# Optimization experiments

Measured on AMD Instinct MI355X. Metric: run time of the kernel, lower is better.

## Reference

```python
import jax, jax.numpy as jnp
import numpy as np


def setup_inputs() -> dict:
    key = jax.random.key(0)
    k1, k2, k3, k4 = jax.random.split(key, 4)
    B, C_in, KH, KW, C_out = 256, 512, 7, 7, 1000
    inputR = jax.random.normal(k1, (B, C_in, KH, KW), dtype=jnp.float32)
    inputSPD = jax.random.normal(k2, (B, C_in, C_in), dtype=jnp.float32)
    fan_in = C_in * KH * KW
    weight = jax.random.normal(k3, (C_out, C_in, KH, KW), dtype=jnp.float32) / np.sqrt(fan_in)
    bias = jax.random.normal(k4, (C_out,), dtype=jnp.float32) / np.sqrt(fan_in)
    return {"inputR": inputR, "inputSPD": inputSPD, "weight": weight, "bias": bias}


def reference(inputR, inputSPD, weight, bias):
    # Conv2d with kernel == spatial size and padding 0 == fully connected layer.
    # outputR: (N, C_out)
    outputR = jnp.einsum('nchw,ochw->no', inputR, weight) + bias

    # top-2 channel selection per sample (indices only; values unused)
    _, top2_idx = jax.lax.top_k(outputR, 2)  # (N, 2)

    # weight is detached for the SPD path in the original module
    w_spd = jax.lax.stop_gradient(weight)[top2_idx]  # (N, 2, C_in, KH, KW)

    # outputSPD[n,k,m] = sum_{c,d,h,w} SPD[n,c,d] * W2[n,k,d,h,w] * W2[n,m,c,h,w]
    # (equivalent to the original's two batched matmuls + sum over (h, w))
    outputSPD = jnp.einsum('ncd,nkdhw,nmchw->nkm', inputSPD, w_spd, w_spd)  # (N, 2, 2)
    return outputR, outputSPD
```

## Files before the change

### kernel.cpp

```cpp
#include <hip/hip_runtime.h>

#define KD 25088
#define N_DIM 1000

typedef __attribute__((ext_vector_type(8))) short bf16x8;
typedef __attribute__((ext_vector_type(4))) float f32x4;

__device__ inline unsigned short f2bf(float x) {
  union { float f; unsigned u; } v; v.f = x;
  unsigned r = v.u + 0x7FFFu + ((v.u >> 16) & 1);
  return (unsigned short)(r >> 16);
}
__device__ inline unsigned pack2(float a, float b) {
  return (unsigned)f2bf(a) | ((unsigned)f2bf(b) << 16);
}
__device__ inline float bf2f(unsigned short u) {
  union { unsigned u; float f; } v; v.u = ((unsigned)u) << 16; return v.f;
}

__global__ __launch_bounds__(256) void init_bias_k(
    const float* __restrict__ bias, float* __restrict__ outR) {
  const int id = blockIdx.x * 256 + threadIdx.x;
  if (id < 256 * N_DIM) outR[id] = bias[id % N_DIM];
}

__global__ __launch_bounds__(256) void rgemm_k(
    const float* __restrict__ A, const float* __restrict__ W,
    float* __restrict__ outR) {
  __shared__ unsigned short As[2][128 * 32];
  __shared__ unsigned short Bs[2][128 * 32];
  const int t = threadIdx.x;
  const int m0 = blockIdx.x * 128;
  const int n0 = blockIdx.y * 128;
  const int z  = blockIdx.z;
  const int lane = t & 63, w = t >> 6;
  const int cw = (w >> 1) * 64, jw = (w & 1) * 64;
  const int r16 = lane & 15, quad = lane >> 4;
  const int srow = t >> 2;
  const int sc8  = (t & 3) << 3;

  float a_pre[16], b_pre[16];

  f32x4 acc[4][4];
#pragma unroll
  for (int i = 0; i < 4; ++i)
#pragma unroll
    for (int j = 0; j < 4; ++j) {
      acc[i][j][0] = 0.f; acc[i][j][1] = 0.f;
      acc[i][j][2] = 0.f; acc[i][j][3] = 0.f;
    }

#define RG_LOAD(s_)                                                         \
  {                                                                         \
    const int kbase = ((z) * 28 + (s_)) * 32;                               \
    _Pragma("unroll")                                                       \
    for (int h = 0; h < 2; ++h) {                                           \
      const int row = h * 64 + srow;                                        \
      const float* pa = A + (size_t)(m0 + row) * KD + kbase + sc8;          \
      *(float4*)&a_pre[h * 8 + 0] = *(const float4*)pa;                     \
      *(float4*)&a_pre[h * 8 + 4] = *(const float4*)(pa + 4);               \
      const int wr = n0 + row;                                              \
      if (wr < N_DIM) {                                                     \
        const float* pw = W + (size_t)wr * KD + kbase + sc8;                \
        *(float4*)&b_pre[h * 8 + 0] = *(const float4*)pw;                   \
        *(float4*)&b_pre[h * 8 + 4] = *(const float4*)(pw + 4);             \
      } else {                                                              \
        _Pragma("unroll")                                                   \
        for (int q = 0; q < 8; ++q) b_pre[h * 8 + q] = 0.f;                 \
      }                                                                     \
    }                                                                       \
  }

#define RG_WRITE(p_)                                                        \
  {                                                                         \
    _Pragma("unroll")                                                       \
    for (int h = 0; h < 2; ++h) {                                           \
      const int row = h * 64 + srow;                                        \
      uint4 ua, ub;                                                         \
      ua.x = pack2(a_pre[h*8+0], a_pre[h*8+1]);                             \
      ua.y = pack2(a_pre[h*8+2], a_pre[h*8+3]);                             \
      ua.z = pack2(a_pre[h*8+4], a_pre[h*8+5]);                             \
      ua.w = pack2(a_pre[h*8+6], a_pre[h*8+7]);                             \
      ub.x = pack2(b_pre[h*8+0], b_pre[h*8+1]);                             \
      ub.y = pack2(b_pre[h*8+2], b_pre[h*8+3]);                             \
      ub.z = pack2(b_pre[h*8+4], b_pre[h*8+5]);                             \
      ub.w = pack2(b_pre[h*8+6], b_pre[h*8+7]);                             \
      *(uint4*)&As[p_][row * 32 + sc8] = ua;                                \
      *(uint4*)&Bs[p_][row * 32 + sc8] = ub;                                \
    }                                                                       \
  }

  RG_LOAD(0); RG_WRITE(0); __syncthreads();
  int p = 0;
  for (int s = 0; s < 28; ++s) {
    if (s + 1 < 28) RG_LOAD(s + 1);
    bf16x8 af[4], bq[4];
#pragma unroll
    for (int i = 0; i < 4; ++i) {
      af[i] = *(const bf16x8*)&As[p][(cw + i * 16 + r16) * 32 + quad * 8];
      bq[i] = *(const bf16x8*)&Bs[p][(jw + i * 16 + r16) * 32 + quad * 8];
    }
#pragma unroll
    for (int i = 0; i < 4; ++i)
#pragma unroll
      for (int j = 0; j < 4; ++j)
        acc[i][j] = __builtin_amdgcn_mfma_f32_16x16x32_bf16(af[i], bq[j], acc[i][j], 0, 0, 0);
    if (s + 1 < 28) RG_WRITE(p ^ 1);
    __syncthreads();
    p ^= 1;
  }

#pragma unroll
  for (int j = 0; j < 4; ++j) {
    const int n = n0 + jw + j * 16 + r16;
    if (n < N_DIM) {
#pragma unroll
      for (int i = 0; i < 4; ++i)
#pragma unroll
        for (int r = 0; r < 4; ++r) {
          const int m = m0 + cw + i * 16 + quad * 4 + r;
          atomicAdd(&outR[(size_t)m * N_DIM + n], acc[i][j][r]);
        }
    }
  }
#undef RG_LOAD
#undef RG_WRITE
}

__global__ __launch_bounds__(64) void top8_k(
    const float* __restrict__ outR, int* __restrict__ top2,
    int* __restrict__ candIdx, int* __restrict__ flags,
    float* __restrict__ outSPD) {
  const int n = blockIdx.x;
  const int lane = threadIdx.x;
  float v[16];
#pragma unroll
  for (int r = 0; r < 16; ++r) {
    const int o = lane + r * 64;
    v[r] = (o < N_DIM) ? outR[n * N_DIM + o] : -3.0e38f;
  }
  float cv[8]; int ci[8];
#pragma unroll
  for (int rr = 0; rr < 8; ++rr) {
    float bv = -3.0e38f; int bi = 0x3fffffff;
#pragma unroll
    for (int r = 0; r < 16; ++r) {
      const int o = lane + r * 64;
      if (v[r] > bv || (v[r] == bv && o < bi)) { bv = v[r]; bi = o; }
    }
#pragma unroll
    for (int off = 32; off >= 1; off >>= 1) {
      const float ov = __shfl_xor(bv, off, 64);
      const int   oi = __shfl_xor(bi, off, 64);
      if (ov > bv || (ov == bv && oi < bi)) { bv = ov; bi = oi; }
    }
    cv[rr] = bv; ci[rr] = bi;
#pragma unroll
    for (int r = 0; r < 16; ++r)
      if (lane + r * 64 == bi) v[r] = -3.0e38f;
  }
  if (lane == 0) {
    const bool safe = (cv[0] - cv[1] >= 0.025f) &&
                      (cv[1] - cv[2] >= 0.025f) &&
                      (cv[1] - cv[7] >= 0.05f);
    flags[n] = safe ? 0 : 1;
    top2[2 * n]     = ci[0];
    top2[2 * n + 1] = ci[1];
#pragma unroll
    for (int r = 0; r < 8; ++r) candIdx[n * 8 + r] = ci[r];
    outSPD[4 * n + 0] = 0.f; outSPD[4 * n + 1] = 0.f;
    outSPD[4 * n + 2] = 0.f; outSPD[4 * n + 3] = 0.f;
  }
}

__global__ __launch_bounds__(256) void rdot_k(
    const float* __restrict__ A, const float* __restrict__ W,
    const float* __restrict__ bias, const int* __restrict__ candIdx,
    const int* __restrict__ flags, float* __restrict__ vals) {
  const int n = blockIdx.x;
  if (!flags[n]) return;
  const int c = blockIdx.y;
  const int idx = candIdx[n * 8 + c];
  const float4* a4 = (const float4*)(A + (size_t)n * KD);
  const float4* w4 = (const float4*)(W + (size_t)idx * KD);
  float s = 0.f;
  for (int i = threadIdx.x; i < KD / 4; i += 256) {
    const float4 av = a4[i];
    const float4 wv = w4[i];
    s += av.x * wv.x + av.y * wv.y + av.z * wv.z + av.w * wv.w;
  }
#pragma unroll
  for (int off = 32; off >= 1; off >>= 1) s += __shfl_xor(s, off, 64);
  __shared__ float red[4];
  const int lane = threadIdx.x & 63, w = threadIdx.x >> 6;
  if (lane == 0) red[w] = s;
  __syncthreads();
  if (threadIdx.x == 0)
    vals[n * 8 + c] = red[0] + red[1] + red[2] + red[3] + bias[idx];
}

__global__ __launch_bounds__(64) void select_k(
    const float* __restrict__ vals, const int* __restrict__ candIdx,
    const int* __restrict__ flags, int* __restrict__ top2) {
  const int n = blockIdx.x;
  if (threadIdx.x != 0 || !flags[n]) return;
  int b0 = -1; float v0 = -3.0e38f; int i0 = 0x3fffffff;
  for (int c = 0; c < 8; ++c) {
    const int idx = candIdx[n * 8 + c];
    const float vv = vals[n * 8 + c];
    if (vv > v0 || (vv == v0 && idx < i0)) { v0 = vv; i0 = idx; b0 = c; }
  }
  float v1 = -3.0e38f; int i1 = 0x3fffffff;
  for (int c = 0; c < 8; ++c) {
    if (c == b0) continue;
    const int idx = candIdx[n * 8 + c];
    const float vv = vals[n * 8 + c];
    if (vv > v1 || (vv == v1 && idx < i1)) { v1 = vv; i1 = idx; }
  }
  top2[2 * n]     = i0;
  top2[2 * n + 1] = i1;
}

__global__ __launch_bounds__(256) void pack_k(
    const float* __restrict__ W, const int* __restrict__ top2,
    unsigned short* __restrict__ Wp) {
  const int n  = blockIdx.x;
  const int jq = blockIdx.y;
  const int ia = top2[2 * n];
  const int ib = top2[2 * n + 1];
  unsigned short* dst = Wp + (size_t)n * 65536;
  for (int u = threadIdx.x; u < 32 * 256; u += 256) {
    const int j  = jq * 32 + (u >> 8);
    const int d2 = (u & 255) * 2;
    unsigned val = 0u;
    if (j < 98) {
      const int kk = (j >= 49);
      const int hw = j - 49 * kk;
      const float* wr = W + (size_t)(kk ? ib : ia) * KD + hw;
      val = pack2(wr[(size_t)d2 * 49], wr[(size_t)(d2 + 1) * 49]);
    }
    *(unsigned*)(dst + j * 512 + d2) = val;
  }
}

__global__ __launch_bounds__(256) void spd_k(
    const float* __restrict__ S, const unsigned short* __restrict__ Wp,
    float* __restrict__ outSPD) {
  __shared__ unsigned short As[2][128 * 32];
  __shared__ unsigned short Bs[2][128 * 32];
  __shared__ float red[4];
  const int t = threadIdx.x;
  const int n  = blockIdx.x >> 2;
  const int c0 = (blockIdx.x & 3) * 128;
  const float* Sn = S + (size_t)n * 512 * 512;
  const unsigned short* Wpn = Wp + (size_t)n * 65536;
  const int lane = t & 63, w = t >> 6;
  const int cw = (w >> 1) * 64, jw = (w & 1) * 64;
  const int r16 = lane & 15, quad = lane >> 4;
  const int srow = t >> 2;
  const int sc8  = (t & 3) << 3;

  if (t < 4) red[t] = 0.f;

  float a_pre[16];
  uint4 b_pre[2];

  f32x4 acc[4][4];
#pragma unroll
  for (int i = 0; i < 4; ++i)
#pragma unroll
    for (int j = 0; j < 4; ++j) {
      acc[i][j][0] = 0.f; acc[i][j][1] = 0.f;
      acc[i][j][2] = 0.f; acc[i][j][3] = 0.f;
    }

#define SP_LOAD(s_)                                                         \
  {                                                                         \
    const int d0 = (s_) * 32;                                               \
    _Pragma("unroll")                                                       \
    for (int h = 0; h < 2; ++h) {                                           \
      const int row = h * 64 + srow;                                        \
      const float* pa = Sn + (size_t)(c0 + row) * 512 + d0 + sc8;           \
      *(float4*)&a_pre[h * 8 + 0] = *(const float4*)pa;                     \
      *(float4*)&a_pre[h * 8 + 4] = *(const float4*)(pa + 4);               \
      b_pre[h] = *(const uint4*)(Wpn + (size_t)row * 512 + d0 + sc8);       \
    }                                                                       \
  }

#define SP_WRITE(p_)                                                        \
  {                                                                         \
    _Pragma("unroll")                                                       \
    for (int h = 0; h < 2; ++h) {                                           \
      const int row = h * 64 + srow;                                        \
      uint4 ua;                                                             \
      ua.x = pack2(a_pre[h*8+0], a_pre[h*8+1]);                             \
      ua.y = pack2(a_pre[h*8+2], a_pre[h*8+3]);                             \
      ua.z = pack2(a_pre[h*8+4], a_pre[h*8+5]);                             \
      ua.w = pack2(a_pre[h*8+6], a_pre[h*8+7]);                             \
      *(uint4*)&As[p_][row * 32 + sc8] = ua;                                \
      *(uint4*)&Bs[p_][row * 32 + sc8] = b_pre[h];                          \
    }                                                                       \
  }

  SP_LOAD(0); SP_WRITE(0); __syncthreads();
  int p = 0;
  for (int s = 0; s < 16; ++s) {
    if (s + 1 < 16) SP_LOAD(s + 1);
    bf16x8 af[4], bq[4];
#pragma unroll
    for (int i = 0; i < 4; ++i) {
      af[i] = *(const bf16x8*)&As[p][(cw + i * 16 + r16) * 32 + quad * 8];
      bq[i] = *(const bf16x8*)&Bs[p][(jw + i * 16 + r16) * 32 + quad * 8];
    }
#pragma unroll
    for (int i = 0; i < 4; ++i)
#pragma unroll
      for (int j = 0; j < 4; ++j)
        acc[i][j] = __builtin_amdgcn_mfma_f32_16x16x32_bf16(af[i], bq[j], acc[i][j], 0, 0, 0);
    if (s + 1 < 16) SP_WRITE(p ^ 1);
    __syncthreads();
    p ^= 1;
  }
#undef SP_LOAD
#undef SP_WRITE

  float p00 = 0.f, p01 = 0.f, p10 = 0.f, p11 = 0.f;
#pragma unroll
  for (int j = 0; j < 4; ++j) {
    const int jj = jw + j * 16 + r16;
    if (jj < 98) {
      const int kk = (jj >= 49);
      const int hw = jj - 49 * kk;
      const unsigned short* wa = Wpn + (size_t)hw * 512;
      const unsigned short* wb = Wpn + (size_t)(49 + hw) * 512;
#pragma unroll
      for (int i = 0; i < 4; ++i) {
#pragma unroll
        for (int r = 0; r < 4; ++r) {
          const int c = c0 + cw + i * 16 + quad * 4 + r;
          const float u   = acc[i][j][r];
          const float wav = bf2f(wa[c]);
          const float wbv = bf2f(wb[c]);
          if (kk == 0) { p00 = fmaf(u, wav, p00); p01 = fmaf(u, wbv, p01); }
          else         { p10 = fmaf(u, wav, p10); p11 = fmaf(u, wbv, p11); }
        }
      }
    }
  }

  atomicAdd(&red[0], p00);
  atomicAdd(&red[1], p01);
  atomicAdd(&red[2], p10);
  atomicAdd(&red[3], p11);
  __syncthreads();
  if (t < 4) atomicAdd(&outSPD[n * 4 + t], red[t]);
}

__global__ __launch_bounds__(256) void spd_fb_k(
    const float* __restrict__ S, const float* __restrict__ W,
    const int* __restrict__ top2, float* __restrict__ outSPD) {
  __shared__ unsigned short As[128 * 40];
  __shared__ unsigned short Bs[128 * 40];
  __shared__ float red[4];
  const int t = threadIdx.x;
  const int n  = blockIdx.x >> 2;
  const int c0 = (blockIdx.x & 3) * 128;
  const int ia = top2[2 * n];
  const int ib = top2[2 * n + 1];
  const float* Sn = S + (size_t)n * 512 * 512;
  const int lane = t & 63, w = t >> 6;
  const int cw = (w >> 1) * 64, jw = (w & 1) * 64;
  const int r16 = lane & 15, quad = lane >> 4;
  if (t < 4) red[t] = 0.f;
  f32x4 acc[4][4];
#pragma unroll
  for (int i = 0; i < 4; ++i)
#pragma unroll
    for (int j = 0; j < 4; ++j) {
      acc[i][j][0] = 0.f; acc[i][j][1] = 0.f;
      acc[i][j][2] = 0.f; acc[i][j][3] = 0.f;
    }
  const int bj  = t & 127;
  const int bh  = t >> 7;
  const int bkk = (bj >= 49);
  const int bhw = bj - 49 * bkk;
  const bool bvalid = (bj < 98);
  const float* brow = W + (size_t)(bkk ? ib : ia) * KD + bhw;
  for (int d0 = 0; d0 < 512; d0 += 32) {
#pragma unroll
    for (int h = 0; h < 4; ++h) {
      const int idx = h * 256 + t;
      const int row = idx >> 3;
      const int c4  = (idx & 7) << 2;
      float4 av = *(const float4*)(Sn + (size_t)(c0 + row) * 512 + d0 + c4);
      uint2 pa;
      pa.x = pack2(av.x, av.y);
      pa.y = pack2(av.z, av.w);
      *(uint2*)&As[row * 40 + c4] = pa;
    }
#pragma unroll
    for (int dd2 = 0; dd2 < 16; dd2 += 2) {
      const int dd = bh * 16 + dd2;
      const float x0 = bvalid ? brow[(size_t)(d0 + dd) * 49] : 0.f;
      const float x1 = bvalid ? brow[(size_t)(d0 + dd + 1) * 49] : 0.f;
      *(unsigned*)&Bs[bj * 40 + dd] = pack2(x0, x1);
    }
    __syncthreads();
    bf16x8 af[4], bq[4];
#pragma unroll
    for (int i = 0; i < 4; ++i) {
      af[i] = *(const bf16x8*)&As[(cw + i * 16 + r16) * 40 + quad * 8];
      bq[i] = *(const bf16x8*)&Bs[(jw + i * 16 + r16) * 40 + quad * 8];
    }
#pragma unroll
    for (int i = 0; i < 4; ++i)
#pragma unroll
      for (int j = 0; j < 4; ++j)
        acc[i][j] = __builtin_amdgcn_mfma_f32_16x16x32_bf16(af[i], bq[j], acc[i][j], 0, 0, 0);
    __syncthreads();
  }
  float p00 = 0.f, p01 = 0.f, p10 = 0.f, p11 = 0.f;
  const float* Wa = W + (size_t)ia * KD;
  const float* Wb = W + (size_t)ib * KD;
#pragma unroll
  for (int j = 0; j < 4; ++j) {
    const int jj = jw + j * 16 + r16;
    if (jj < 98) {
      const int kk = (jj >= 49);
      const int hw = jj - 49 * kk;
#pragma unroll
      for (int i = 0; i < 4; ++i)
#pragma unroll
        for (int r = 0; r < 4; ++r) {
          const int c = c0 + cw + i * 16 + quad * 4 + r;
          const float u  = acc[i][j][r];
          const float wa = Wa[(size_t)c * 49 + hw];
          const float wb = Wb[(size_t)c * 49 + hw];
          if (kk == 0) { p00 = fmaf(u, wa, p00); p01 = fmaf(u, wb, p01); }
          else         { p10 = fmaf(u, wa, p10); p11 = fmaf(u, wb, p11); }
        }
    }
  }
  atomicAdd(&red[0], p00);
  atomicAdd(&red[1], p01);
  atomicAdd(&red[2], p10);
  atomicAdd(&red[3], p11);
  __syncthreads();
  if (t < 4) atomicAdd(&outSPD[n * 4 + t], red[t]);
}

extern "C" void kernel_launch(void* const* d_in, const int* in_sizes, int n_in,
                              void* d_out, int out_size, void* d_ws, size_t ws_size,
                              hipStream_t stream) {
  const float* inputR   = (const float*)d_in[0];
  const float* inputSPD = (const float*)d_in[1];
  const float* weight   = (const float*)d_in[2];
  const float* bias     = (const float*)d_in[3];
  float* out = (float*)d_out;

  int*   top2    = (int*)d_ws;
  int*   candIdx = (int*)((char*)d_ws + 2048);
  int*   flags   = (int*)((char*)d_ws + 2048 + 8192);
  float* vals    = (float*)((char*)d_ws + 2048 + 8192 + 1024);
  unsigned short* Wp = (unsigned short*)((char*)d_ws + 65536);
  const bool bigws = ws_size >= 65536ull + 256ull * 65536ull * 2ull;

  init_bias_k<<<dim3(1000), 256, 0, stream>>>(bias, out);
  rgemm_k<<<dim3(2, 8, 28), 256, 0, stream>>>(inputR, weight, out);
  top8_k<<<dim3(256), 64, 0, stream>>>(out, top2, candIdx, flags, out + 256000);
  rdot_k<<<dim3(256, 8), 256, 0, stream>>>(inputR, weight, bias, candIdx, flags, vals);
  select_k<<<dim3(256), 64, 0, stream>>>(vals, candIdx, flags, top2);
  if (bigws) {
    pack_k<<<dim3(256, 4), 256, 0, stream>>>(weight, top2, Wp);
    spd_k<<<dim3(1024), 256, 0, stream>>>(inputSPD, Wp, out + 256000);
  } else {
    spd_fb_k<<<dim3(1024), 256, 0, stream>>>(inputSPD, weight, top2, out + 256000);
  }
}
```

Before: 660.5 us.

## Replace split-K atomics with partial buffers and fuse selection into weight packing

Result: faster. 635.1 us (-3.9%).

```diff
diff --git a/kernel.cpp b/kernel.cpp
--- a/kernel.cpp
+++ b/kernel.cpp
@@ -2,6 +2,7 @@
 
 #define KD 25088
 #define N_DIM 1000
+#define ZS 28
 
 typedef __attribute__((ext_vector_type(8))) short bf16x8;
 typedef __attribute__((ext_vector_type(4))) float f32x4;
@@ -24,9 +25,10 @@
   if (id < 256 * N_DIM) outR[id] = bias[id % N_DIM];
 }
 
+template<int ATOMIC>
 __global__ __launch_bounds__(256) void rgemm_k(
     const float* __restrict__ A, const float* __restrict__ W,
-    float* __restrict__ outR) {
+    float* __restrict__ D) {
   __shared__ unsigned short As[2][128 * 32];
   __shared__ unsigned short Bs[2][128 * 32];
   const int t = threadIdx.x;
@@ -52,7 +54,7 @@
 
 #define RG_LOAD(s_)                                                         \
   {                                                                         \
-    const int kbase = ((z) * 28 + (s_)) * 32;                               \
+    const int kbase = ((z) * ZS + (s_)) * 32;                               \
     _Pragma("unroll")                                                       \
     for (int h = 0; h < 2; ++h) {                                           \
       const int row = h * 64 + srow;                                        \
@@ -92,8 +94,8 @@
 
   RG_LOAD(0); RG_WRITE(0); __syncthreads();
   int p = 0;
-  for (int s = 0; s < 28; ++s) {
-    if (s + 1 < 28) RG_LOAD(s + 1);
+  for (int s = 0; s < ZS; ++s) {
+    if (s + 1 < ZS) RG_LOAD(s + 1);
     bf16x8 af[4], bq[4];
 #pragma unroll
     for (int i = 0; i < 4; ++i) {
@@ -105,7 +107,7 @@
 #pragma unroll
       for (int j = 0; j < 4; ++j)
         acc[i][j] = __builtin_amdgcn_mfma_f32_16x16x32_bf16(af[i], bq[j], acc[i][j], 0, 0, 0);
-    if (s + 1 < 28) RG_WRITE(p ^ 1);
+    if (s + 1 < ZS) RG_WRITE(p ^ 1);
     __syncthreads();
     p ^= 1;
   }
@@ -119,7 +121,10 @@
 #pragma unroll
         for (int r = 0; r < 4; ++r) {
           const int m = m0 + cw + i * 16 + quad * 4 + r;
-          atomicAdd(&outR[(size_t)m * N_DIM + n], acc[i][j][r]);
+          if (ATOMIC)
+            atomicAdd(&D[(size_t)m * N_DIM + n], acc[i][j][r]);
+          else
+            D[((size_t)z * 256 + m) * N_DIM + n] = acc[i][j][r];
         }
     }
   }
@@ -127,17 +132,40 @@
 #undef RG_WRITE
 }
 
+template<int FROMPART>
 __global__ __launch_bounds__(64) void top8_k(
-    const float* __restrict__ outR, int* __restrict__ top2,
+    const float* __restrict__ src, const float* __restrict__ bias,
+    float* __restrict__ outR, int* __restrict__ top2,
     int* __restrict__ candIdx, int* __restrict__ flags,
     float* __restrict__ outSPD) {
   const int n = blockIdx.x;
   const int lane = threadIdx.x;
   float v[16];
-#pragma unroll
-  for (int r = 0; r < 16; ++r) {
-    const int o = lane + r * 64;
-    v[r] = (o < N_DIM) ? outR[n * N_DIM + o] : -3.0e38f;
+  if (FROMPART) {
+#pragma unroll
+    for (int r = 0; r < 16; ++r) {
+      const int o = lane + r * 64;
+      v[r] = (o < N_DIM) ? bias[o] : -3.0e38f;
+    }
+    for (int z = 0; z < ZS; ++z) {
+      const float* pz = src + ((size_t)z * 256 + n) * N_DIM;
+#pragma unroll
+      for (int r = 0; r < 16; ++r) {
+        const int o = lane + r * 64;
+        if (o < N_DIM) v[r] += pz[o];
+      }
+    }
+#pragma unroll
+    for (int r = 0; r < 16; ++r) {
+      const int o = lane + r * 64;
+      if (o < N_DIM) outR[(size_t)n * N_DIM + o] = v[r];
+    }
+  } else {
+#pragma unroll
+    for (int r = 0; r < 16; ++r) {
+      const int o = lane + r * 64;
+      v[r] = (o < N_DIM) ? src[(size_t)n * N_DIM + o] : -3.0e38f;
+    }
   }
   float cv[8]; int ci[8];
 #pragma unroll
@@ -221,25 +249,76 @@
   top2[2 * n + 1] = i1;
 }
 
-__global__ __launch_bounds__(256) void pack_k(
-    const float* __restrict__ W, const int* __restrict__ top2,
+__global__ __launch_bounds__(256) void packsel_k(
+    const float* __restrict__ W, const int* __restrict__ candIdx,
+    const int* __restrict__ flags, const float* __restrict__ vals,
     unsigned short* __restrict__ Wp) {
-  const int n  = blockIdx.x;
-  const int jq = blockIdx.y;
-  const int ia = top2[2 * n];
-  const int ib = top2[2 * n + 1];
-  unsigned short* dst = Wp + (size_t)n * 65536;
-  for (int u = threadIdx.x; u < 32 * 256; u += 256) {
-    const int j  = jq * 32 + (u >> 8);
-    const int d2 = (u & 255) * 2;
-    unsigned val = 0u;
-    if (j < 98) {
-      const int kk = (j >= 49);
-      const int hw = j - 49 * kk;
-      const float* wr = W + (size_t)(kk ? ib : ia) * KD + hw;
-      val = pack2(wr[(size_t)d2 * 49], wr[(size_t)(d2 + 1) * 49]);
-    }
-    *(unsigned*)(dst + j * 512 + d2) = val;
+  __shared__ unsigned short tile[49 * 130];
+  __shared__ int sel_s;
+  const int n = blockIdx.x;
+  const int which = blockIdx.y;
+  const int t = threadIdx.x;
+  if (t == 0) {
+    int ia, ib;
+    if (!flags[n]) {
+      ia = candIdx[n * 8];
+      ib = candIdx[n * 8 + 1];
+    } else {
+      int b0 = -1; float v0 = -3.0e38f; int i0 = 0x3fffffff;
+      for (int c = 0; c < 8; ++c) {
+        const int idx = candIdx[n * 8 + c];
+        const float vv = vals[n * 8 + c];
+        if (vv > v0 || (vv == v0 && idx < i0)) { v0 = vv; i0 = idx; b0 = c; }
+      }
+      float v1 = -3.0e38f; int i1 = 0x3fffffff;
+      for (int c = 0; c < 8; ++c) {
+        if (c == b0) continue;
+        const int idx = candIdx[n * 8 + c];
+        const float vv = vals[n * 8 + c];
+        if (vv > v1 || (vv == v1 && idx < i1)) { v1 = vv; i1 = idx; }
+      }
+      ia = i0; ib = i1;
+    }
+    sel_s = which ? ib : ia;
+  }
+  unsigned short* dstn = Wp + (size_t)n * 65536;
+  {
+    const int r0 = 98 + which * 15;
+    for (int u = t; u < 15 * 128; u += 256) {
+      const int rr = u >> 7;
+      const int cc = (u & 127) << 1;
+      *(unsigned*)(dstn + (size_t)(r0 + rr) * 512 + cc) = 0u;
+    }
+  }
+  __syncthreads();
+  const int sel = sel_s;
+  const float4* src4 = (const float4*)(W + (size_t)sel * KD);
+  for (int chunk = 0; chunk < 4; ++chunk) {
+    const float4* s4 = src4 + chunk * 1568;
+    for (int u4 = t; u4 < 1568; u4 += 256) {
+      const float4 fv = s4[u4];
+      const float vv[4] = {fv.x, fv.y, fv.z, fv.w};
+      const int i0 = u4 * 4;
+#pragma unroll
+      for (int e = 0; e < 4; ++e) {
+        const int idx = i0 + e;
+        const int c = idx / 49;
+        const int hw = idx - c * 49;
+        tile[hw * 130 + c] = f2bf(vv[e]);
+      }
+    }
+    __syncthreads();
+    const int cp = t & 63, hwb = t >> 6;
+    unsigned short* wbase = dstn + (size_t)which * 49 * 512 + chunk * 128 + 2 * cp;
+#pragma unroll
+    for (int it = 0; it < 13; ++it) {
+      const int hw = hwb + it * 4;
+      if (hw < 49) {
+        const unsigned val = *(const unsigned*)&tile[hw * 130 + 2 * cp];
+        *(unsigned*)(wbase + (size_t)hw * 512) = val;
+      }
+    }
+    __syncthreads();
   }
 }
 
@@ -462,18 +541,23 @@
   int*   candIdx = (int*)((char*)d_ws + 2048);
   int*   flags   = (int*)((char*)d_ws + 2048 + 8192);
   float* vals    = (float*)((char*)d_ws + 2048 + 8192 + 1024);
-  unsigned short* Wp = (unsigned short*)((char*)d_ws + 65536);
-  const bool bigws = ws_size >= 65536ull + 256ull * 65536ull * 2ull;
-
-  init_bias_k<<<dim3(1000), 256, 0, stream>>>(bias, out);
-  rgemm_k<<<dim3(2, 8, 28), 256, 0, stream>>>(inputR, weight, out);
-  top8_k<<<dim3(256), 64, 0, stream>>>(out, top2, candIdx, flags, out + 256000);
-  rdot_k<<<dim3(256, 8), 256, 0, stream>>>(inputR, weight, bias, candIdx, flags, vals);
-  select_k<<<dim3(256), 64, 0, stream>>>(vals, candIdx, flags, top2);
+  float* part    = (float*)((char*)d_ws + 65536);
+  const size_t PART_BYTES = (size_t)ZS * 256 * N_DIM * 4;
+  unsigned short* Wp = (unsigned short*)((char*)d_ws + 65536 + PART_BYTES);
+  const bool bigws = ws_size >= 65536ull + PART_BYTES + 256ull * 65536ull * 2ull;
+
   if (bigws) {
-    pack_k<<<dim3(256, 4), 256, 0, stream>>>(weight, top2, Wp);
+    rgemm_k<0><<<dim3(2, 8, ZS), 256, 0, stream>>>(inputR, weight, part);
+    top8_k<1><<<dim3(256), 64, 0, stream>>>(part, bias, out, top2, candIdx, flags, out + 256000);
+    rdot_k<<<dim3(256, 8), 256, 0, stream>>>(inputR, weight, bias, candIdx, flags, vals);
+    packsel_k<<<dim3(256, 2), 256, 0, stream>>>(weight, candIdx, flags, vals, Wp);
     spd_k<<<dim3(1024), 256, 0, stream>>>(inputSPD, Wp, out + 256000);
   } else {
+    init_bias_k<<<dim3(1000), 256, 0, stream>>>(bias, out);
+    rgemm_k<1><<<dim3(2, 8, ZS), 256, 0, stream>>>(inputR, weight, out);
+    top8_k<0><<<dim3(256), 64, 0, stream>>>(out, bias, out, top2, candIdx, flags, out + 256000);
+    rdot_k<<<dim3(256, 8), 256, 0, stream>>>(inputR, weight, bias, candIdx, flags, vals);
+    select_k<<<dim3(256), 64, 0, stream>>>(vals, candIdx, flags, top2);
     spd_fb_k<<<dim3(1024), 256, 0, stream>>>(inputSPD, weight, top2, out + 256000);
   }
 }
```
